# Optimization experiments

Hardware: AMD Instinct MI355X
Metric: run time of the kernel (lower is better)

## Reference

```python
import jax, jax.numpy as jnp
import numpy as np

D_MODEL = 1024
H = 16
D_K = D_MODEL // H


def setup_inputs() -> dict:
    key = jax.random.key(0)
    ks = jax.random.split(key, 12)
    B, S = 2, 2048
    scale = 1.0 / np.sqrt(D_MODEL)
    inp = {
        "q": jax.random.normal(ks[0], (B, S, D_MODEL), jnp.float32),
        "k": jax.random.normal(ks[1], (B, S, D_MODEL), jnp.float32),
        "v": jax.random.normal(ks[2], (B, S, D_MODEL), jnp.float32),
        "mask": jnp.ones((B, 1, S, S), jnp.int32),
        # nn.Linear weights are [out, in]; applied as x @ W.T + b
        "Wq": jax.random.normal(ks[3], (D_MODEL, D_MODEL), jnp.float32) * scale,
        "bq": jnp.zeros((D_MODEL,), jnp.float32),
        "Wk": jax.random.normal(ks[4], (D_MODEL, D_MODEL), jnp.float32) * scale,
        "bk": jnp.zeros((D_MODEL,), jnp.float32),
        "Wv": jax.random.normal(ks[5], (D_MODEL, D_MODEL), jnp.float32) * scale,
        "bv": jnp.zeros((D_MODEL,), jnp.float32),
        "Wo": jax.random.normal(ks[6], (D_MODEL, D_MODEL), jnp.float32) * scale,
        "bo": jnp.zeros((D_MODEL,), jnp.float32),
    }
    return inp


def reference(q, k, v, mask, Wq, bq, Wk, bk, Wv, bv, Wo, bo):
    B, S, _ = q.shape
    # projections
    query = q @ Wq.T + bq
    key_ = k @ Wk.T + bk
    value = v @ Wv.T + bv
    # [B, S, D] -> [B, H, S, d_k]
    query = query.reshape(B, S, H, D_K).transpose(0, 2, 1, 3)
    key_ = key_.reshape(B, S, H, D_K).transpose(0, 2, 1, 3)
    value = value.reshape(B, S, H, D_K).transpose(0, 2, 1, 3)
    # scaled dot-product attention with full [B,H,S,S] scores (as in source)
    scores = jnp.einsum("bhqd,bhkd->bhqk", query, key_) / jnp.sqrt(
        jnp.asarray(D_K, query.dtype)
    )
    # NOTE: source uses masked_fill value = -1e-09 (faithful reproduction)
    scores = jnp.where(mask == 0, jnp.asarray(-1e-09, scores.dtype), scores)
    attn = jax.nn.softmax(scores, axis=-1)
    # dropout p=0.0 -> identity
    x = jnp.einsum("bhqk,bhkd->bhqd", attn, value)
    x = x.transpose(0, 2, 1, 3).reshape(B, S, H * D_K)
    return x @ Wo.T + bo
```

## Files before the change

### kernel.cpp

```cpp
#include <hip/hip_runtime.h>
#include <hip/hip_bf16.h>
#include <stdint.h>

#define DI __device__ __forceinline__

typedef __bf16 bf16x8 __attribute__((ext_vector_type(8)));
typedef __bf16 bf16x4 __attribute__((ext_vector_type(4)));
typedef float  f32x4  __attribute__((ext_vector_type(4)));

constexpr int Bc = 2, Sc = 2048, Dm = 1024, Hc = 16;
constexpr int Mrows = Bc * Sc;
constexpr float LOG2E = 1.4426950408889634f;

DI void async16(void* lds, const void* g) {
  __builtin_amdgcn_global_load_lds(
      (const __attribute__((address_space(1))) void*)g,
      (__attribute__((address_space(3))) void*)lds, 16, 0, 0);
}

DI void cvt_one(const float* __restrict__ in, __bf16* __restrict__ out, int i) {
  const f32x4* in4 = (const f32x4*)in;
  f32x4 a = in4[2 * i], b = in4[2 * i + 1];
  bf16x8 o;
#pragma unroll
  for (int j = 0; j < 4; ++j) { o[j] = (__bf16)a[j]; o[4 + j] = (__bf16)b[j]; }
  ((bf16x8*)out)[i] = o;
}

__global__ void cvt3(const float* __restrict__ a, const float* __restrict__ b,
                     const float* __restrict__ c, __bf16* __restrict__ oa,
                     __bf16* __restrict__ ob, __bf16* __restrict__ oc, int n8) {
  int i = blockIdx.x * blockDim.x + threadIdx.x;
  if (i >= n8) return;
  cvt_one(a, oa, i); cvt_one(b, ob, i); cvt_one(c, oc, i);
}

__global__ void cvt4(const float* __restrict__ a, const float* __restrict__ b,
                     const float* __restrict__ c, const float* __restrict__ d,
                     __bf16* __restrict__ oa, __bf16* __restrict__ ob,
                     __bf16* __restrict__ oc, __bf16* __restrict__ od, int n8) {
  int i = blockIdx.x * blockDim.x + threadIdx.x;
  if (i >= n8) return;
  cvt_one(a, oa, i); cvt_one(b, ob, i); cvt_one(c, oc, i); cvt_one(d, od, i);
}

__global__ void pack_mask(const int* __restrict__ m, unsigned long long* __restrict__ bits) {
  const int total = Bc * Sc * Sc;
  const int nth = gridDim.x * blockDim.x;
  for (int i = blockIdx.x * blockDim.x + threadIdx.x; i < total; i += nth) {
    unsigned long long b = __ballot(m[i] != 0);
    if ((threadIdx.x & 63) == 0) bits[i >> 6] = b;
  }
}

DI void gemm_core(const __bf16* __restrict__ A, const __bf16* __restrict__ Bw,
                  __bf16* As, __bf16* Bs, int m0, int n0, int t, f32x4 (&acc)[4][4]) {
  const int lane = t & 63, wv = t >> 6;
  const int lo = lane & 15, hi = lane >> 4;
  const int wm = (wv >> 1) * 64, wn = (wv & 1) * 64;
  const int rowA = t >> 2, kc8 = (t & 3) * 8;

  auto stage = [&](int buf, int k0) {
    __bf16* as = As + buf * 4096;
    __bf16* bs = Bs + buf * 4096;
    async16(&as[t * 8],        A  + (size_t)(m0 + rowA) * 1024      + k0 + kc8);
    async16(&as[t * 8 + 2048], A  + (size_t)(m0 + rowA + 64) * 1024 + k0 + kc8);
    async16(&bs[t * 8],        Bw + (size_t)(n0 + rowA) * 1024      + k0 + kc8);
    async16(&bs[t * 8 + 2048], Bw + (size_t)(n0 + rowA + 64) * 1024 + k0 + kc8);
  };

  stage(0, 0);
  __syncthreads();
  int cur = 0;
  for (int k0 = 0; k0 < 1024; k0 += 32) {
    if (k0 + 32 < 1024) stage(cur ^ 1, k0 + 32);
    const __bf16* as = As + cur * 4096;
    const __bf16* bs = Bs + cur * 4096;
    bf16x8 af[4], bfr[4];
#pragma unroll
    for (int i = 0; i < 4; ++i)
      af[i] = *(const bf16x8*)&as[(wm + i * 16 + lo) * 32 + hi * 8];
#pragma unroll
    for (int j = 0; j < 4; ++j)
      bfr[j] = *(const bf16x8*)&bs[(wn + j * 16 + lo) * 32 + hi * 8];
#pragma unroll
    for (int i = 0; i < 4; ++i)
#pragma unroll
      for (int j = 0; j < 4; ++j)
        acc[i][j] = __builtin_amdgcn_mfma_f32_16x16x32_bf16(af[i], bfr[j], acc[i][j], 0, 0, 0);
    __syncthreads();
    cur ^= 1;
  }
}

__global__ __launch_bounds__(256, 3)
void gemm_qkv(const __bf16* __restrict__ Aq, const __bf16* __restrict__ Ak,
              const __bf16* __restrict__ Av, const __bf16* __restrict__ Wqb,
              const __bf16* __restrict__ Wkb, const __bf16* __restrict__ Wvb,
              const float* __restrict__ bq, const float* __restrict__ bk,
              const float* __restrict__ bv,
              __bf16* __restrict__ Qh, __bf16* __restrict__ Kh, __bf16* __restrict__ Vt) {
  __shared__ __bf16 As[2][128 * 32];
  __shared__ __bf16 Bs[2][128 * 32];
  const int which = blockIdx.x >> 8;
  int local = blockIdx.x & 255;
  local = (local & 7) * 32 + (local >> 3);
  const int m0 = (local >> 3) * 128, n0 = (local & 7) * 128;
  const __bf16* A    = which == 0 ? Aq  : which == 1 ? Ak  : Av;
  const __bf16* Bw   = which == 0 ? Wqb : which == 1 ? Wkb : Wvb;
  const float*  bias = which == 0 ? bq  : which == 1 ? bk  : bv;
  const int t = threadIdx.x;

  f32x4 acc[4][4] = {};
  gemm_core(A, Bw, &As[0][0], &Bs[0][0], m0, n0, t, acc);

  const int lane = t & 63, wv = t >> 6, lo = lane & 15, hi = lane >> 4;
  const int wm = (wv >> 1) * 64, wn = (wv & 1) * 64;

  if (which < 2) {
    __bf16* C = which ? Kh : Qh;
#pragma unroll
    for (int mi = 0; mi < 4; ++mi) {
      const int mbase = m0 + wm + mi * 16 + hi * 4;
      const int b = mbase >> 11, s = mbase & 2047;
#pragma unroll
      for (int ni = 0; ni < 4; ++ni) {
        const int n = n0 + wn + ni * 16 + lo;
        const int h = n >> 6, d = n & 63;
        const float bb = bias[n];
        __bf16* p = C + ((size_t)(b * Hc + h) * Sc + s) * 64 + d;
#pragma unroll
        for (int r = 0; r < 4; ++r)
          p[(size_t)r * 64] = (__bf16)(acc[mi][ni][r] + bb);
      }
    }
  } else {
#pragma unroll
    for (int mi = 0; mi < 4; ++mi) {
      const int mbase = m0 + wm + mi * 16 + hi * 4;
      const int b = mbase >> 11, s0 = mbase & 2047;
#pragma unroll
      for (int ni = 0; ni < 4; ++ni) {
        const int n = n0 + wn + ni * 16 + lo;
        const int h = n >> 6, d = n & 63;
        const float bb = bias[n];
        bf16x4 pk;
#pragma unroll
        for (int r = 0; r < 4; ++r) pk[r] = (__bf16)(acc[mi][ni][r] + bb);
        *(bf16x4*)(Vt + ((size_t)(b * Hc + h) * 64 + d) * Sc + s0) = pk;
      }
    }
  }
}

__global__ __launch_bounds__(256, 3)
void gemm_o(const __bf16* __restrict__ A, const __bf16* __restrict__ Bw,
            const float* __restrict__ bias, float* __restrict__ C) {
  __shared__ __bf16 As[2][128 * 32];
  __shared__ __bf16 Bs[2][128 * 32];
  int bid = blockIdx.x;
  bid = (bid & 7) * 32 + (bid >> 3);
  const int m0 = (bid >> 3) * 128, n0 = (bid & 7) * 128;
  const int t = threadIdx.x;

  f32x4 acc[4][4] = {};
  gemm_core(A, Bw, &As[0][0], &Bs[0][0], m0, n0, t, acc);

  const int lane = t & 63, wv = t >> 6, lo = lane & 15, hi = lane >> 4;
  const int wm = (wv >> 1) * 64, wn = (wv & 1) * 64;
#pragma unroll
  for (int mi = 0; mi < 4; ++mi) {
    const int mbase = m0 + wm + mi * 16 + hi * 4;
#pragma unroll
    for (int ni = 0; ni < 4; ++ni) {
      const int n = n0 + wn + ni * 16 + lo;
      const float bb = bias[n];
#pragma unroll
      for (int r = 0; r < 4; ++r)
        C[(size_t)(mbase + r) * 1024 + n] = acc[mi][ni][r] + bb;
    }
  }
}

__global__ __launch_bounds__(512, 4)
void attn_fwd(const __bf16* __restrict__ Qh, const __bf16* __restrict__ Kh,
              const __bf16* __restrict__ Vt, const unsigned long long* __restrict__ mbits,
              __bf16* __restrict__ X) {
  __shared__ __bf16 Ks[2][64 * 64];
  __shared__ __bf16 Vs[2][64 * 64];
  __shared__ __bf16 Pq[8][16][72];

  int bid = blockIdx.x;
  bid = (bid & 7) * 64 + (bid >> 3);
  const int qblk = bid & 15, h = (bid >> 4) & 15, b = bid >> 8;
  const int t = threadIdx.x, lane = t & 63, wv = t >> 6;
  const int lo = lane & 15, hi = lane >> 4;
  const int q0 = qblk * 128 + wv * 16;

  const size_t headoff = (size_t)(b * Hc + h) * Sc * 64;
  const __bf16* Qp = Qh + headoff + (size_t)q0 * 64;
  const __bf16* Kp = Kh + headoff;
  const __bf16* Vp = Vt + headoff;

  bf16x8 qf[2];
#pragma unroll
  for (int c = 0; c < 2; ++c)
    qf[c] = *(const bf16x8*)&Qp[lo * 64 + c * 32 + hi * 8];

  f32x4 o[4] = {};
  float mr = -1e30f, lr = 0.f;

  const int srow = t >> 3, scb = t & 7;
  const int ksrc = ((scb ^ (srow & 7)) * 8);

  auto stage = [&](int buf, int kb) {
    async16(&Ks[buf][t * 8], Kp + (size_t)(kb + srow) * 64 + ksrc);
    async16(&Vs[buf][t * 8], Vp + (size_t)srow * Sc + kb + ksrc);
  };

  stage(0, 0);
  int cur = 0;
  const int xr = (lo & 7) << 3;
  const unsigned long long* mrow = mbits + (size_t)(b * Sc + q0 + lo) * (Sc / 64);

  for (int kb = 0; kb < Sc; kb += 64) {
    __syncthreads();
    if (kb + 64 < Sc) stage(cur ^ 1, kb + 64);

    f32x4 sc[4];
    __builtin_amdgcn_s_setprio(1);
#pragma unroll
    for (int kc = 0; kc < 4; ++kc) {
      bf16x8 kf0 = *(const bf16x8*)&Ks[cur][(kc * 16 + lo) * 64 + ((hi * 8) ^ xr)];
      bf16x8 kf1 = *(const bf16x8*)&Ks[cur][(kc * 16 + lo) * 64 + ((32 + hi * 8) ^ xr)];
      f32x4 z = {0.f, 0.f, 0.f, 0.f};
      sc[kc] = __builtin_amdgcn_mfma_f32_16x16x32_bf16(kf0, qf[0], z, 0, 0, 0);
      sc[kc] = __builtin_amdgcn_mfma_f32_16x16x32_bf16(kf1, qf[1], sc[kc], 0, 0, 0);
    }
    __builtin_amdgcn_s_setprio(0);

    const unsigned long long mb = mrow[kb >> 6];
    const bool allm = __all(mb == ~0ull);
    float pvv[4][4];
#pragma unroll
    for (int kc = 0; kc < 4; ++kc)
#pragma unroll
      for (int r = 0; r < 4; ++r) pvv[kc][r] = sc[kc][r] * 0.125f;
    if (!allm) {
#pragma unroll
      for (int kc = 0; kc < 4; ++kc)
#pragma unroll
        for (int r = 0; r < 4; ++r)
          if (!((mb >> (kc * 16 + hi * 4 + r)) & 1ull)) pvv[kc][r] = -1e-9f;
    }
    float pmax = -1e30f;
#pragma unroll
    for (int kc = 0; kc < 4; ++kc)
#pragma unroll
      for (int r = 0; r < 4; ++r) pmax = fmaxf(pmax, pvv[kc][r]);
    pmax = fmaxf(pmax, __shfl_xor(pmax, 16));
    pmax = fmaxf(pmax, __shfl_xor(pmax, 32));

    if (!__all(pmax <= mr + 8.f)) {
      const float mn = fmaxf(mr, pmax);
      const float fs = exp2f((mr - mn) * LOG2E);
      lr *= fs;
#pragma unroll
      for (int d0 = 0; d0 < 4; ++d0) o[d0] *= fs;
      mr = mn;
    }
    const float mj = mr * LOG2E;
    float rs = 0.f;
#pragma unroll
    for (int kc = 0; kc < 4; ++kc)
#pragma unroll
      for (int r = 0; r < 4; ++r) {
        const float p = exp2f(__builtin_fmaf(pvv[kc][r], LOG2E, -mj));
        pvv[kc][r] = p; rs += p;
      }
    rs += __shfl_xor(rs, 16);
    rs += __shfl_xor(rs, 32);
    lr += rs;

#pragma unroll
    for (int kc = 0; kc < 4; ++kc) {
      bf16x4 pk;
#pragma unroll
      for (int r = 0; r < 4; ++r) pk[r] = (__bf16)pvv[kc][r];
      *(bf16x4*)&Pq[wv][lo][kc * 16 + hi * 4] = pk;
    }

    bf16x8 pa[2];
#pragma unroll
    for (int c = 0; c < 2; ++c)
      pa[c] = *(const bf16x8*)&Pq[wv][lo][c * 32 + hi * 8];
    __builtin_amdgcn_s_setprio(1);
#pragma unroll
    for (int d0 = 0; d0 < 4; ++d0) {
      bf16x8 vf0 = *(const bf16x8*)&Vs[cur][(d0 * 16 + lo) * 64 + ((hi * 8) ^ xr)];
      bf16x8 vf1 = *(const bf16x8*)&Vs[cur][(d0 * 16 + lo) * 64 + ((32 + hi * 8) ^ xr)];
      o[d0] = __builtin_amdgcn_mfma_f32_16x16x32_bf16(vf0, pa[0], o[d0], 0, 0, 0);
      o[d0] = __builtin_amdgcn_mfma_f32_16x16x32_bf16(vf1, pa[1], o[d0], 0, 0, 0);
    }
    __builtin_amdgcn_s_setprio(0);
    cur ^= 1;
  }

  const float inv = 1.f / lr;
#pragma unroll
  for (int d0 = 0; d0 < 4; ++d0) {
    bf16x4 st;
#pragma unroll
    for (int r = 0; r < 4; ++r) st[r] = (__bf16)(o[d0][r] * inv);
    *(bf16x4*)&X[(size_t)(b * Sc + q0 + lo) * 1024 + h * 64 + d0 * 16 + hi * 4] = st;
  }
}

extern "C" void kernel_launch(void* const* d_in, const int* in_sizes, int n_in,
                              void* d_out, int out_size, void* d_ws, size_t ws_size,
                              hipStream_t stream) {
  const float* q  = (const float*)d_in[0];
  const float* k  = (const float*)d_in[1];
  const float* v  = (const float*)d_in[2];
  const int*   mask = (const int*)d_in[3];
  const float* Wq = (const float*)d_in[4];
  const float* bq = (const float*)d_in[5];
  const float* Wk = (const float*)d_in[6];
  const float* bk = (const float*)d_in[7];
  const float* Wv = (const float*)d_in[8];
  const float* bv = (const float*)d_in[9];
  const float* Wo = (const float*)d_in[10];
  const float* bo = (const float*)d_in[11];

  const size_t MB = 1u << 20;
  if (ws_size < 66 * MB) return;

  char* ws = (char*)d_ws;
  __bf16* wqb  = (__bf16*)(ws + 0 * MB);
  __bf16* wkb  = (__bf16*)(ws + 2 * MB);
  __bf16* wvb  = (__bf16*)(ws + 4 * MB);
  __bf16* wob  = (__bf16*)(ws + 6 * MB);
  __bf16* qbin = (__bf16*)(ws + 8 * MB);
  __bf16* kbin = (__bf16*)(ws + 16 * MB);
  __bf16* vbin = (__bf16*)(ws + 24 * MB);
  __bf16* Qh   = (__bf16*)(ws + 32 * MB);
  __bf16* Kh   = (__bf16*)(ws + 40 * MB);
  __bf16* Vt   = (__bf16*)(ws + 48 * MB);
  __bf16* Xat  = (__bf16*)(ws + 56 * MB);
  unsigned long long* mbits = (unsigned long long*)(ws + 64 * MB);

  const int nIn8 = Mrows * Dm / 8;
  const int nW8  = Dm * Dm / 8;
  cvt3<<<nIn8 / 256, 256, 0, stream>>>(q, k, v, qbin, kbin, vbin, nIn8);
  cvt4<<<nW8 / 256, 256, 0, stream>>>(Wq, Wk, Wv, Wo, wqb, wkb, wvb, wob, nW8);
  pack_mask<<<4096, 256, 0, stream>>>(mask, mbits);

  gemm_qkv<<<768, 256, 0, stream>>>(qbin, kbin, vbin, wqb, wkb, wvb, bq, bk, bv, Qh, Kh, Vt);

  attn_fwd<<<512, 512, 0, stream>>>(Qh, Kh, Vt, mbits, Xat);

  gemm_o<<<256, 256, 0, stream>>>(Xat, wob, bo, (float*)d_out);
}
```

Before: 284.5 us.

## Drop LDS staging of K/V in attention, load fragments directly from global

The attention kernel no longer double-buffers K and V tiles through shared memory with async loads and block barriers. Each wave now reads its K and V MFMA fragments straight from global memory (relying on L2/cache reuse across the 8 waves), which removes the per-iteration __syncthreads. The 1/sqrt(d_k) scale is folded into the Q projection epilogue, and the occupancy hints for all kernels are raised. The risk is redundant global traffic and exposed memory latency, since nothing prefetches the next tile.

```diff
diff --git a/kernel.cpp b/kernel.cpp
--- a/kernel.cpp
+++ b/kernel.cpp
@@ -93,7 +93,7 @@
   }
 }
 
-__global__ __launch_bounds__(256, 3)
+__global__ __launch_bounds__(256, 4)
 void gemm_qkv(const __bf16* __restrict__ Aq, const __bf16* __restrict__ Ak,
               const __bf16* __restrict__ Av, const __bf16* __restrict__ Wqb,
               const __bf16* __restrict__ Wkb, const __bf16* __restrict__ Wvb,
@@ -119,6 +119,7 @@
 
   if (which < 2) {
     __bf16* C = which ? Kh : Qh;
+    const float scl = which == 0 ? 0.125f : 1.0f;
 #pragma unroll
     for (int mi = 0; mi < 4; ++mi) {
       const int mbase = m0 + wm + mi * 16 + hi * 4;
@@ -131,7 +132,7 @@
         __bf16* p = C + ((size_t)(b * Hc + h) * Sc + s) * 64 + d;
 #pragma unroll
         for (int r = 0; r < 4; ++r)
-          p[(size_t)r * 64] = (__bf16)(acc[mi][ni][r] + bb);
+          p[(size_t)r * 64] = (__bf16)((acc[mi][ni][r] + bb) * scl);
       }
     }
   } else {
@@ -153,7 +154,7 @@
   }
 }
 
-__global__ __launch_bounds__(256, 3)
+__global__ __launch_bounds__(256, 4)
 void gemm_o(const __bf16* __restrict__ A, const __bf16* __restrict__ Bw,
             const float* __restrict__ bias, float* __restrict__ C) {
   __shared__ __bf16 As[2][128 * 32];
@@ -182,14 +183,11 @@
   }
 }
 
-__global__ __launch_bounds__(512, 4)
+__global__ __launch_bounds__(512, 8)
 void attn_fwd(const __bf16* __restrict__ Qh, const __bf16* __restrict__ Kh,
               const __bf16* __restrict__ Vt, const unsigned long long* __restrict__ mbits,
               __bf16* __restrict__ X) {
-  __shared__ __bf16 Ks[2][64 * 64];
-  __shared__ __bf16 Vs[2][64 * 64];
-  __shared__ __bf16 Pq[8][16][72];
-
+  __shared__ __bf16 Pq[8][16][68];
   int bid = blockIdx.x;
   bid = (bid & 7) * 64 + (bid >> 3);
   const int qblk = bid & 15, h = (bid >> 4) & 15, b = bid >> 8;
@@ -209,30 +207,16 @@
 
   f32x4 o[4] = {};
   float mr = -1e30f, lr = 0.f;
-
-  const int srow = t >> 3, scb = t & 7;
-  const int ksrc = ((scb ^ (srow & 7)) * 8);
-
-  auto stage = [&](int buf, int kb) {
-    async16(&Ks[buf][t * 8], Kp + (size_t)(kb + srow) * 64 + ksrc);
-    async16(&Vs[buf][t * 8], Vp + (size_t)srow * Sc + kb + ksrc);
-  };
-
-  stage(0, 0);
-  int cur = 0;
-  const int xr = (lo & 7) << 3;
   const unsigned long long* mrow = mbits + (size_t)(b * Sc + q0 + lo) * (Sc / 64);
 
   for (int kb = 0; kb < Sc; kb += 64) {
-    __syncthreads();
-    if (kb + 64 < Sc) stage(cur ^ 1, kb + 64);
-
     f32x4 sc[4];
     __builtin_amdgcn_s_setprio(1);
 #pragma unroll
     for (int kc = 0; kc < 4; ++kc) {
-      bf16x8 kf0 = *(const bf16x8*)&Ks[cur][(kc * 16 + lo) * 64 + ((hi * 8) ^ xr)];
-      bf16x8 kf1 = *(const bf16x8*)&Ks[cur][(kc * 16 + lo) * 64 + ((32 + hi * 8) ^ xr)];
+      const __bf16* kr = Kp + (size_t)(kb + kc * 16 + lo) * 64 + hi * 8;
+      bf16x8 kf0 = *(const bf16x8*)kr;
+      bf16x8 kf1 = *(const bf16x8*)(kr + 32);
       f32x4 z = {0.f, 0.f, 0.f, 0.f};
       sc[kc] = __builtin_amdgcn_mfma_f32_16x16x32_bf16(kf0, qf[0], z, 0, 0, 0);
       sc[kc] = __builtin_amdgcn_mfma_f32_16x16x32_bf16(kf1, qf[1], sc[kc], 0, 0, 0);
@@ -240,24 +224,18 @@
     __builtin_amdgcn_s_setprio(0);
 
     const unsigned long long mb = mrow[kb >> 6];
-    const bool allm = __all(mb == ~0ull);
-    float pvv[4][4];
+    if (!__all(mb == ~0ull)) {
+#pragma unroll
+      for (int kc = 0; kc < 4; ++kc)
+#pragma unroll
+        for (int r = 0; r < 4; ++r)
+          if (!((mb >> (kc * 16 + hi * 4 + r)) & 1ull)) sc[kc][r] = -1e-9f;
+    }
+    float pmax = -1e30f;
 #pragma unroll
     for (int kc = 0; kc < 4; ++kc)
 #pragma unroll
-      for (int r = 0; r < 4; ++r) pvv[kc][r] = sc[kc][r] * 0.125f;
-    if (!allm) {
-#pragma unroll
-      for (int kc = 0; kc < 4; ++kc)
-#pragma unroll
-        for (int r = 0; r < 4; ++r)
-          if (!((mb >> (kc * 16 + hi * 4 + r)) & 1ull)) pvv[kc][r] = -1e-9f;
-    }
-    float pmax = -1e30f;
-#pragma unroll
-    for (int kc = 0; kc < 4; ++kc)
-#pragma unroll
-      for (int r = 0; r < 4; ++r) pmax = fmaxf(pmax, pvv[kc][r]);
+      for (int r = 0; r < 4; ++r) pmax = fmaxf(pmax, sc[kc][r]);
     pmax = fmaxf(pmax, __shfl_xor(pmax, 16));
     pmax = fmaxf(pmax, __shfl_xor(pmax, 32));
 
@@ -275,8 +253,8 @@
     for (int kc = 0; kc < 4; ++kc)
 #pragma unroll
       for (int r = 0; r < 4; ++r) {
-        const float p = exp2f(__builtin_fmaf(pvv[kc][r], LOG2E, -mj));
-        pvv[kc][r] = p; rs += p;
+        const float p = exp2f(__builtin_fmaf(sc[kc][r], LOG2E, -mj));
+        sc[kc][r] = p; rs += p;
       }
     rs += __shfl_xor(rs, 16);
     rs += __shfl_xor(rs, 32);
@@ -286,24 +264,22 @@
     for (int kc = 0; kc < 4; ++kc) {
       bf16x4 pk;
 #pragma unroll
-      for (int r = 0; r < 4; ++r) pk[r] = (__bf16)pvv[kc][r];
+      for (int r = 0; r < 4; ++r) pk[r] = (__bf16)sc[kc][r];
       *(bf16x4*)&Pq[wv][lo][kc * 16 + hi * 4] = pk;
     }
-
-    bf16x8 pa[2];
-#pragma unroll
-    for (int c = 0; c < 2; ++c)
-      pa[c] = *(const bf16x8*)&Pq[wv][lo][c * 32 + hi * 8];
+    bf16x8 pa0 = *(const bf16x8*)&Pq[wv][lo][hi * 8];
+    bf16x8 pa1 = *(const bf16x8*)&Pq[wv][lo][32 + hi * 8];
+
     __builtin_amdgcn_s_setprio(1);
 #pragma unroll
     for (int d0 = 0; d0 < 4; ++d0) {
-      bf16x8 vf0 = *(const bf16x8*)&Vs[cur][(d0 * 16 + lo) * 64 + ((hi * 8) ^ xr)];
-      bf16x8 vf1 = *(const bf16x8*)&Vs[cur][(d0 * 16 + lo) * 64 + ((32 + hi * 8) ^ xr)];
-      o[d0] = __builtin_amdgcn_mfma_f32_16x16x32_bf16(vf0, pa[0], o[d0], 0, 0, 0);
-      o[d0] = __builtin_amdgcn_mfma_f32_16x16x32_bf16(vf1, pa[1], o[d0], 0, 0, 0);
+      const __bf16* vr = Vp + (size_t)(d0 * 16 + lo) * Sc + kb + hi * 8;
+      bf16x8 vf0 = *(const bf16x8*)vr;
+      bf16x8 vf1 = *(const bf16x8*)(vr + 32);
+      o[d0] = __builtin_amdgcn_mfma_f32_16x16x32_bf16(vf0, pa0, o[d0], 0, 0, 0);
+      o[d0] = __builtin_amdgcn_mfma_f32_16x16x32_bf16(vf1, pa1, o[d0], 0, 0, 0);
     }
     __builtin_amdgcn_s_setprio(0);
-    cur ^= 1;
   }
 
   const float inv = 1.f / lr;
```

New measurement: 455.7 us. 1.6x slower.
